# Kernel tuning notes

Hardware: AMD Instinct MI355X
Metric: run time of the kernel (lower is better)

The kernel has to match this reference:

```python
import jax, jax.numpy as jnp
import numpy as np

B, S, HID = 1, 2048, 2048
H, HD, DR = 16, 128, 64
CKV, CQ = 512, 1536
ROPE_BASE = 10000.0


def _rope_cos_sin(seq_len, dim, dtype):
    inv_freq = 1.0 / (ROPE_BASE ** (jnp.arange(0, dim, 2, dtype=jnp.float32) / dim))
    t = jnp.arange(seq_len, dtype=jnp.float32)
    freqs = jnp.outer(t, inv_freq)                      # [S, DR/2]
    emb = jnp.concatenate([freqs, freqs], axis=-1)      # [S, DR]
    return jnp.cos(emb).astype(dtype), jnp.sin(emb).astype(dtype)


def _rotate_half(x):
    x1, x2 = jnp.split(x, 2, axis=-1)
    return jnp.concatenate([-x2, x1], axis=-1)


def _xavier(key, fan_in, fan_out):
    lim = np.sqrt(6.0 / (fan_in + fan_out))
    return jax.random.uniform(key, (fan_in, fan_out), jnp.float32, -lim, lim)


def setup_inputs() -> dict:
    key = jax.random.key(0)
    ks = jax.random.split(key, 10)
    hidden_states = jax.random.normal(ks[0], (B, S, HID), jnp.float32)
    # causal mask: 1.0 where position is masked out (j > i)
    mask = jnp.triu(jnp.ones((S, S), jnp.float32), k=1)[None, None]  # [1,1,S,S]
    return {
        "hidden_states": hidden_states,
        "mask": mask,
        "W_DKV": _xavier(ks[1], HID, CKV),
        "W_UK": _xavier(ks[2], CKV, H * HD),
        "W_UV": _xavier(ks[3], CKV, H * HD),
        "W_DQ": _xavier(ks[4], HID, CQ),
        "W_UQ": _xavier(ks[5], CQ, H * HD),
        "W_QR": _xavier(ks[6], CQ, H * DR),
        "W_KR": _xavier(ks[7], HID, DR),
        "W_O": _xavier(ks[8], H * HD, HID),
    }


def reference(hidden_states, mask, W_DKV, W_UK, W_UV, W_DQ, W_UQ, W_QR, W_KR, W_O):
    b, s, _ = hidden_states.shape
    scale = 1.0 / np.sqrt(HD + DR)

    c_KV = hidden_states @ W_DKV                         # [B,S,CKV]
    k_C = (c_KV @ W_UK).reshape(b, s, H, HD)
    v = (c_KV @ W_UV).reshape(b, s, H, HD)
    c_Q = hidden_states @ W_DQ                           # [B,S,CQ]
    q_C = (c_Q @ W_UQ).reshape(b, s, H, HD)
    q_R = (c_Q @ W_QR).reshape(b, s, H, DR)
    k_R = (hidden_states @ W_KR).reshape(b, s, 1, DR)

    cos, sin = _rope_cos_sin(s, DR, hidden_states.dtype)
    cos = cos[None, :, None, :]                          # [1,S,1,DR]
    sin = sin[None, :, None, :]
    q_R = q_R * cos + _rotate_half(q_R) * sin
    k_R = k_R * cos + _rotate_half(k_R) * sin            # [B,S,1,DR], broadcast over heads

    q = jnp.concatenate([q_C, q_R], axis=-1)             # [B,S,H,HD+DR]
    k = jnp.concatenate([k_C, jnp.broadcast_to(k_R, (b, s, H, DR))], axis=-1)

    # [B,H,Sq,Sk]
    scores = jnp.einsum("bqhd,bkhd->bhqk", q, k) * scale
    if mask is not None:
        scores = scores + mask * -1e9                     # broadcast over heads
    probs = jax.nn.softmax(scores, axis=-1)
    out = jnp.einsum("bhqk,bkhd->bqhd", probs, v).reshape(b, s, H * HD)
    return out @ W_O
```

## Files before the change

### kernel.cpp

```cpp
#include <hip/hip_runtime.h>
#include <hip/hip_bf16.h>
#include <math.h>

typedef __hip_bfloat16 bf16;
typedef short s16x8 __attribute__((ext_vector_type(8)));
typedef unsigned short u16x8 __attribute__((ext_vector_type(8)));
typedef float f32x4 __attribute__((ext_vector_type(4)));

#define S_LEN 2048
#define NHEAD 16
#define HDIM  128
#define DROT  64

__device__ __forceinline__ float bf2f(unsigned short u) {
    union { unsigned int i; float f; } v;
    v.i = ((unsigned int)u) << 16;
    return v.f;
}
__device__ __forceinline__ unsigned short f2bf(float f) {
    union { float f; unsigned int i; } v;
    v.f = f;
    unsigned int r = (v.i + 0x7FFFu + ((v.i >> 16) & 1u)) >> 16;
    return (unsigned short)r;
}

__device__ __forceinline__ void load_lds16(const unsigned short* g, unsigned short* l) {
    __builtin_amdgcn_global_load_lds(
        (const __attribute__((address_space(1))) unsigned short*)g,
        (__attribute__((address_space(3))) unsigned short*)l, 16, 0, 0);
}

__device__ __forceinline__ bool is_bf16(const unsigned int* maskw) {
    return maskw[1] != 0x3F800000u;
}

struct PrepDesc {
    const void* in;
    unsigned short* out;
    int R, C, blk_start, nbx, kind;
};
struct PrepBatch { PrepDesc d[8]; };

__global__ __launch_bounds__(256)
void prep_kernel(PrepBatch b, const unsigned int* __restrict__ maskw) {
    const bool fb = is_bf16(maskw);
    __shared__ unsigned short t[64][80];
    PrepDesc dd = b.d[0];
    #pragma unroll
    for (int p = 1; p < 8; ++p)
        if ((int)blockIdx.x >= b.d[p].blk_start) dd = b.d[p];
    const int local = (int)blockIdx.x - dd.blk_start;
    const int tid = threadIdx.x;

    if (dd.kind == 1) {
        const size_t idx = ((size_t)local * 256 + tid) * 8;
        if (fb) {
            *(u16x8*)(dd.out + idx) = *(const u16x8*)((const unsigned short*)dd.in + idx);
        } else {
            const float* p = (const float*)dd.in + idx;
            float4 f0 = *(const float4*)p;
            float4 f1 = *(const float4*)(p + 4);
            u16x8 u;
            u[0] = f2bf(f0.x); u[1] = f2bf(f0.y); u[2] = f2bf(f0.z); u[3] = f2bf(f0.w);
            u[4] = f2bf(f1.x); u[5] = f2bf(f1.y); u[6] = f2bf(f1.z); u[7] = f2bf(f1.w);
            *(u16x8*)(dd.out + idx) = u;
        }
        return;
    }

    const int by = local / dd.nbx, bx = local - by * dd.nbx;
    const int r0 = by << 6, c0 = bx << 6;
    const int tr = tid >> 3;
    const int tc8 = (tid & 7) << 3;
    #pragma unroll
    for (int p = 0; p < 2; ++p) {
        const int r = tr + p * 32;
        const size_t off = (size_t)(r0 + r) * dd.C + c0 + tc8;
        unsigned short v[8];
        if (fb) {
            u16x8 u = *(const u16x8*)((const unsigned short*)dd.in + off);
            #pragma unroll
            for (int j = 0; j < 8; ++j) v[j] = u[j];
        } else {
            const float* p4 = (const float*)dd.in + off;
            float4 f0 = *(const float4*)p4;
            float4 f1 = *(const float4*)(p4 + 4);
            v[0] = f2bf(f0.x); v[1] = f2bf(f0.y); v[2] = f2bf(f0.z); v[3] = f2bf(f0.w);
            v[4] = f2bf(f1.x); v[5] = f2bf(f1.y); v[6] = f2bf(f1.z); v[7] = f2bf(f1.w);
        }
        #pragma unroll
        for (int j = 0; j < 8; ++j) t[tc8 + j][r] = v[j];
    }
    __syncthreads();
    #pragma unroll
    for (int p = 0; p < 2; ++p) {
        const int c = tr + p * 32;
        u16x8 u = *(const u16x8*)&t[c][tc8];
        *(u16x8*)(dd.out + (size_t)(c0 + c) * dd.R + r0 + tc8) = u;
    }
}

__global__ __launch_bounds__(256)
void transpose_conv(const void* __restrict__ in, unsigned short* __restrict__ out,
                    int R, int C, const unsigned int* __restrict__ maskw) {
    const bool fb = is_bf16(maskw);
    __shared__ unsigned short t[64][80];
    const int r0 = blockIdx.y << 6, c0 = blockIdx.x << 6;
    const int tid = threadIdx.x;
    const int tr = tid >> 3;
    const int tc8 = (tid & 7) << 3;
    #pragma unroll
    for (int p = 0; p < 2; ++p) {
        const int r = tr + p * 32;
        const size_t off = (size_t)(r0 + r) * C + c0 + tc8;
        unsigned short v[8];
        if (fb) {
            u16x8 u = *(const u16x8*)((const unsigned short*)in + off);
            #pragma unroll
            for (int j = 0; j < 8; ++j) v[j] = u[j];
        } else {
            const float* p4 = (const float*)in + off;
            float4 f0 = *(const float4*)p4;
            float4 f1 = *(const float4*)(p4 + 4);
            v[0] = f2bf(f0.x); v[1] = f2bf(f0.y); v[2] = f2bf(f0.z); v[3] = f2bf(f0.w);
            v[4] = f2bf(f1.x); v[5] = f2bf(f1.y); v[6] = f2bf(f1.z); v[7] = f2bf(f1.w);
        }
        #pragma unroll
        for (int j = 0; j < 8; ++j) t[tc8 + j][r] = v[j];
    }
    __syncthreads();
    #pragma unroll
    for (int p = 0; p < 2; ++p) {
        const int c = tr + p * 32;
        u16x8 u = *(const u16x8*)&t[c][tc8];
        *(u16x8*)(out + (size_t)(c0 + c) * R + r0 + tc8) = u;
    }
}

struct GemmDesc {
    const unsigned short* A;
    const unsigned short* Bt;
    void* C;
    int M, N, K;
    int nbx;
    int blk_start;
    int ct;
};
struct GemmBatch { GemmDesc d[4]; };

template <int NP, int CMODE>
__global__ __launch_bounds__(256)
void mfma_gemm2(GemmBatch batch, const unsigned int* __restrict__ maskw) {
    __shared__ __align__(16) unsigned short As[128 * 32];
    __shared__ __align__(16) unsigned short Bs[128 * 32];

    GemmDesc dd = batch.d[0];
    #pragma unroll
    for (int p = 1; p < NP; ++p)
        if ((int)blockIdx.x >= batch.d[p].blk_start) dd = batch.d[p];
    const int local = (int)blockIdx.x - dd.blk_start;
    const int by = local / dd.nbx;
    const int bx = local - by * dd.nbx;
    const int m0 = by << 7, n0 = bx << 7;
    const int K = dd.K;

    const int tid  = threadIdx.x;
    const int lane = tid & 63;
    const int w    = tid >> 6;
    const int wr = w >> 1, wc = w & 1;
    const int l15 = lane & 15, quad = lane >> 4, q8 = quad << 3;

    int srow[2], scol[2];
    #pragma unroll
    for (int i = 0; i < 2; ++i) {
        const int c = (2 * w + i) * 64 + lane;
        srow[i] = c >> 2;
        scol[i] = (c & 3) << 3;
    }

    f32x4 acc[4][4];
    #pragma unroll
    for (int i = 0; i < 4; ++i)
        #pragma unroll
        for (int j = 0; j < 4; ++j) {
            f32x4 z = {0.f, 0.f, 0.f, 0.f};
            acc[i][j] = z;
        }

    for (int k0 = 0; k0 < K; k0 += 32) {
        __syncthreads();
        #pragma unroll
        for (int i = 0; i < 2; ++i) {
            load_lds16(dd.A  + (size_t)(m0 + srow[i]) * K + k0 + scol[i],
                       As + (2 * w + i) * 512);
            load_lds16(dd.Bt + (size_t)(n0 + srow[i]) * K + k0 + scol[i],
                       Bs + (2 * w + i) * 512);
        }
        __syncthreads();
        s16x8 af[4], bf[4];
        #pragma unroll
        for (int mt = 0; mt < 4; ++mt)
            af[mt] = *(const s16x8*)&As[(wr * 64 + mt * 16 + l15) * 32 + q8];
        #pragma unroll
        for (int nt = 0; nt < 4; ++nt)
            bf[nt] = *(const s16x8*)&Bs[(wc * 64 + nt * 16 + l15) * 32 + q8];
        #pragma unroll
        for (int nt = 0; nt < 4; ++nt)
            #pragma unroll
            for (int mt = 0; mt < 4; ++mt)
                acc[mt][nt] = __builtin_amdgcn_mfma_f32_16x16x32_bf16(
                    af[mt], bf[nt], acc[mt][nt], 0, 0, 0);
    }

    bool cbf = true;
    if (CMODE == 2) cbf = is_bf16(maskw);
    const int M = dd.M, N = dd.N;
    #pragma unroll
    for (int mt = 0; mt < 4; ++mt)
        #pragma unroll
        for (int nt = 0; nt < 4; ++nt) {
            f32x4 d = acc[mt][nt];
            const int col  = n0 + wc * 64 + nt * 16 + l15;
            const int rowb = m0 + wr * 64 + mt * 16 + quad * 4;
            if (dd.ct) {
                ushort4 o;
                o.x = f2bf(d[0]); o.y = f2bf(d[1]); o.z = f2bf(d[2]); o.w = f2bf(d[3]);
                *(ushort4*)((unsigned short*)dd.C + (size_t)col * M + rowb) = o;
            } else if (cbf) {
                unsigned short* c = (unsigned short*)dd.C + (size_t)rowb * N + col;
                #pragma unroll
                for (int r = 0; r < 4; ++r) c[(size_t)r * N] = f2bf(d[r]);
            } else {
                float* c = (float*)dd.C + (size_t)rowb * N + col;
                #pragma unroll
                for (int r = 0; r < 4; ++r) c[(size_t)r * N] = d[r];
            }
        }
}

__global__ __launch_bounds__(256)
void rope_all(unsigned short* __restrict__ qR, unsigned short* __restrict__ kRb) {
    int bid = blockIdx.x;
    unsigned short* x;
    int nh, stride;
    if (bid < 4096) { x = qR; nh = 16; stride = 64; }
    else            { x = kRb; nh = 1; stride = 128; bid -= 4096; }
    const int idx = bid * 256 + threadIdx.x;
    const int d = idx & 31;
    const int rest = idx >> 5;
    const int h = rest % nh;
    const int s = rest / nh;
    if (s >= S_LEN) return;
    const float inv = powf(10000.0f, -(float)d * (1.0f / 32.0f));
    const float ang = (float)s * inv;
    float si, co;
    sincosf(ang, &si, &co);
    unsigned short* p = x + ((size_t)s * nh + h) * stride;
    const float x1 = bf2f(p[d]);
    const float x2 = bf2f(p[d + 32]);
    p[d]      = f2bf(x1 * co - x2 * si);
    p[d + 32] = f2bf(x2 * co + x1 * si);
}

__global__ __launch_bounds__(256)
void mfma_attn(const unsigned short* __restrict__ qC,
               const unsigned short* __restrict__ qR,
               const unsigned short* __restrict__ kC,
               const unsigned short* __restrict__ kRb,
               const unsigned short* __restrict__ vT,
               unsigned short* __restrict__ at) {
    __shared__ __align__(16) struct {
        unsigned short Ks[64][200];
        unsigned short Vs[128][72];
        unsigned short Ps[4][16][72];
    } sm;

    const int tid  = threadIdx.x;
    const int lane = tid & 63;
    const int w    = tid >> 6;
    const int l15 = lane & 15, quad = lane >> 4, q8 = quad << 3;

    const int bid  = (int)blockIdx.x;
    const int half = bid >> 8;
    const int idx  = bid & 255;
    const int h    = idx & 15;
    const int qh   = idx >> 4;
    const int qb   = half ? (31 - qh) : qh;
    const int q0 = qb << 6;
    const int qrow = q0 + w * 16 + l15;

    s16x8 qf[6];
    {
        const unsigned short* qCrow = qC + ((size_t)qrow * NHEAD + h) * HDIM;
        #pragma unroll
        for (int s = 0; s < 4; ++s)
            qf[s] = *(const s16x8*)(qCrow + s * 32 + q8);
        const unsigned short* qRrow = qR + ((size_t)qrow * NHEAD + h) * DROT;
        #pragma unroll
        for (int s = 0; s < 2; ++s)
            qf[4 + s] = *(const s16x8*)(qRrow + s * 32 + q8);
    }

    f32x4 accO[8];
    #pragma unroll
    for (int i = 0; i < 8; ++i) { f32x4 z = {0.f, 0.f, 0.f, 0.f}; accO[i] = z; }
    float slocal[4] = {0.f, 0.f, 0.f, 0.f};

    const float scale = 0.0721687836487032f;
    const int ntiles = (q0 >> 6) + 1;

    const int krow = tid >> 2, kcb = (tid & 3) * 48;
    const int vd = tid >> 1, vcb = (tid & 1) << 5;

    u16x8 kreg[6], vreg[4];
    {
        #pragma unroll
        for (int m = 0; m < 6; ++m) {
            const int c = kcb + m * 8;
            const unsigned short* src = (c < 128)
                ? kC + ((size_t)krow * NHEAD + h) * HDIM + c
                : kRb + (size_t)krow * 128 + (c - 128);
            kreg[m] = *(const u16x8*)src;
        }
        const unsigned short* vrow = vT + (size_t)(h * HDIM + vd) * S_LEN;
        #pragma unroll
        for (int m = 0; m < 4; ++m)
            vreg[m] = *(const u16x8*)(vrow + vcb + m * 8);
    }

    for (int t = 0; t < ntiles; ++t) {
        const int key0 = t << 6;
        __syncthreads();
        #pragma unroll
        for (int m = 0; m < 6; ++m)
            *(u16x8*)&sm.Ks[krow][kcb + m * 8] = kreg[m];
        #pragma unroll
        for (int m = 0; m < 4; ++m)
            *(u16x8*)&sm.Vs[vd][vcb + m * 8] = vreg[m];
        __syncthreads();

        if (t + 1 < ntiles) {
            const int kn = key0 + 64;
            #pragma unroll
            for (int m = 0; m < 6; ++m) {
                const int c = kcb + m * 8;
                const unsigned short* src = (c < 128)
                    ? kC + ((size_t)(kn + krow) * NHEAD + h) * HDIM + c
                    : kRb + (size_t)(kn + krow) * 128 + (c - 128);
                kreg[m] = *(const u16x8*)src;
            }
            const unsigned short* vrow = vT + (size_t)(h * HDIM + vd) * S_LEN + kn;
            #pragma unroll
            for (int m = 0; m < 4; ++m)
                vreg[m] = *(const u16x8*)(vrow + vcb + m * 8);
        }

        f32x4 sA[4];
        #pragma unroll
        for (int nt = 0; nt < 4; ++nt) { f32x4 z = {0.f, 0.f, 0.f, 0.f}; sA[nt] = z; }
        #pragma unroll
        for (int s = 0; s < 6; ++s)
            #pragma unroll
            for (int nt = 0; nt < 4; ++nt) {
                s16x8 kf = *(const s16x8*)&sm.Ks[nt * 16 + l15][s * 32 + q8];
                sA[nt] = __builtin_amdgcn_mfma_f32_16x16x32_bf16(qf[s], kf, sA[nt], 0, 0, 0);
            }

        const int rbase = q0 + w * 16 + quad * 4;
        const bool diag = (key0 + 63 > q0 + w * 16);
        float pv[4][4];
        #pragma unroll
        for (int nt = 0; nt < 4; ++nt) {
            const int col = key0 + nt * 16 + l15;
            #pragma unroll
            for (int r = 0; r < 4; ++r) {
                float s = sA[nt][r] * scale;
                if (diag && (col > rbase + r)) s = -1e30f;
                pv[nt][r] = __expf(s);
            }
        }
        #pragma unroll
        for (int r = 0; r < 4; ++r) {
            slocal[r] += (pv[0][r] + pv[1][r]) + (pv[2][r] + pv[3][r]);
            #pragma unroll
            for (int nt = 0; nt < 4; ++nt)
                sm.Ps[w][quad * 4 + r][nt * 16 + l15] = f2bf(pv[nt][r]);
        }

        s16x8 pf0 = *(const s16x8*)&sm.Ps[w][l15][q8];
        s16x8 pf1 = *(const s16x8*)&sm.Ps[w][l15][32 + q8];
        #pragma unroll
        for (int dt = 0; dt < 8; ++dt) {
            s16x8 vf0 = *(const s16x8*)&sm.Vs[dt * 16 + l15][q8];
            s16x8 vf1 = *(const s16x8*)&sm.Vs[dt * 16 + l15][32 + q8];
            accO[dt] = __builtin_amdgcn_mfma_f32_16x16x32_bf16(pf0, vf0, accO[dt], 0, 0, 0);
            accO[dt] = __builtin_amdgcn_mfma_f32_16x16x32_bf16(pf1, vf1, accO[dt], 0, 0, 0);
        }
    }

    float l_r[4];
    #pragma unroll
    for (int r = 0; r < 4; ++r) {
        float sum = slocal[r];
        #pragma unroll
        for (int off = 1; off < 16; off <<= 1)
            sum += __shfl_xor(sum, off, 64);
        l_r[r] = sum;
    }

    #pragma unroll
    for (int r = 0; r < 4; ++r) {
        const float linv = 1.f / l_r[r];
        const int row = q0 + w * 16 + quad * 4 + r;
        unsigned short* dst = at + (size_t)row * (NHEAD * HDIM) + h * HDIM + l15;
        #pragma unroll
        for (int dt = 0; dt < 8; ++dt)
            dst[dt * 16] = f2bf(accO[dt][r] * linv);
    }
}

extern "C" void kernel_launch(void* const* d_in, const int* in_sizes, int n_in,
                              void* d_out, int out_size, void* d_ws, size_t ws_size,
                              hipStream_t stream) {
    (void)in_sizes; (void)n_in; (void)out_size; (void)ws_size;

    const void* hs    = d_in[0];
    const unsigned int* maskw = (const unsigned int*)d_in[1];
    const void* W_DKV = d_in[2];
    const void* W_UK  = d_in[3];
    const void* W_UV  = d_in[4];
    const void* W_DQ  = d_in[5];
    const void* W_UQ  = d_in[6];
    const void* W_QR  = d_in[7];
    const void* W_KR  = d_in[8];
    const void* W_O   = d_in[9];

    const size_t M1 = 1048576;
    unsigned short* ws    = (unsigned short*)d_ws;
    unsigned short* cKV   = ws;
    unsigned short* cQ    = ws + 1 * M1;
    unsigned short* kC    = ws + 4 * M1;
    unsigned short* vT    = ws + 8 * M1;
    unsigned short* DKVt  = ws + 8 * M1;
    unsigned short* DQt   = ws + 9 * M1;
    unsigned short* qC    = ws + 12 * M1;
    unsigned short* hs_bf = ws + 12 * M1;
    unsigned short* qR    = ws + 16 * M1;
    unsigned short* kRb   = ws + 18 * M1;
    unsigned short* KRt   = ws + 18 * M1 + 262144;
    unsigned short* at    = ws + 18 * M1 + 524288;
    unsigned short* UKt   = at;
    unsigned short* UVt   = at + 1 * M1;
    unsigned short* QRt   = at + 2 * M1;
    unsigned short* UQt   = ws + 22 * M1 + 524288;
    unsigned short* WOt   = ws;

    const dim3 blk(256);

    {
        PrepBatch b{};
        b.d[0] = { hs,    hs_bf, 0, 0,           0,  0, 1 };
        b.d[1] = { W_DKV, DKVt,  2048,  512,  2048,  8, 0 };
        b.d[2] = { W_DQ,  DQt,   2048, 1536,  2304, 24, 0 };
        b.d[3] = { W_KR,  KRt,   2048,   64,  3072,  1, 0 };
        b.d[4] = { W_UK,  UKt,    512, 2048,  3104, 32, 0 };
        b.d[5] = { W_UV,  UVt,    512, 2048,  3360, 32, 0 };
        b.d[6] = { W_UQ,  UQt,   1536, 2048,  3616, 32, 0 };
        b.d[7] = { W_QR,  QRt,   1536, 1024,  4384, 16, 0 };
        prep_kernel<<<4768, blk, 0, stream>>>(b, maskw);
    }

    {
        GemmBatch b{};
        b.d[0] = { hs_bf, DQt,  (void*)cQ,  2048, 1536, 2048, 12,   0, 0 };
        b.d[1] = { hs_bf, DKVt, (void*)cKV, 2048,  512, 2048,  4, 192, 0 };
        b.d[2] = { hs_bf, KRt,  (void*)kRb, 2048,  128, 2048,  1, 256, 0 };
        b.d[3] = b.d[2];
        mfma_gemm2<3, 1><<<272, blk, 0, stream>>>(b, maskw);
    }

    {
        GemmBatch b{};
        b.d[0] = { cQ,  UQt, (void*)qC, 2048, 2048, 1536, 16,   0, 0 };
        b.d[1] = { cQ,  QRt, (void*)qR, 2048, 1024, 1536,  8, 256, 0 };
        b.d[2] = { cKV, UKt, (void*)kC, 2048, 2048,  512, 16, 384, 0 };
        b.d[3] = { cKV, UVt, (void*)vT, 2048, 2048,  512, 16, 640, 1 };
        mfma_gemm2<4, 1><<<896, blk, 0, stream>>>(b, maskw);
    }

    rope_all<<<4352, blk, 0, stream>>>(qR, kRb);

    transpose_conv<<<dim3(32, 32), blk, 0, stream>>>(W_O, WOt, 2048, 2048, maskw);

    mfma_attn<<<512, blk, 0, stream>>>(qC, qR, kC, kRb, vT, at);

    {
        GemmBatch b{};
        b.d[0] = { at, WOt, d_out, 2048, 2048, 2048, 16, 0, 0 };
        b.d[1] = b.d[0]; b.d[2] = b.d[0]; b.d[3] = b.d[0];
        mfma_gemm2<1, 2><<<256, blk, 0, stream>>>(b, maskw);
    }
}
```

Baseline: 356.4 us.

## Split attention waves 2x2 over query and key halves with LDS reduction

Reorganizes the attention block so each wave handles 32 query rows and 32 keys of every 64-key tile, instead of 16 rows against all 64 keys. Each K and V fragment read from LDS is now reused for two MFMAs, cutting LDS traffic per MFMA. Waves whose key half lies entirely above the causal diagonal skip that tile. The two key-half partial outputs and row sums are combined through a shared-memory union at the end, which adds an extra sync and a reduction pass and doubles the per-wave accumulator registers, possibly lowering occupancy.

Result: no change. 361.8 us (+1.5%).

```diff
diff --git a/kernel.cpp b/kernel.cpp
--- a/kernel.cpp
+++ b/kernel.cpp
@@ -269,42 +269,54 @@
                const unsigned short* __restrict__ kRb,
                const unsigned short* __restrict__ vT,
                unsigned short* __restrict__ at) {
-    __shared__ __align__(16) struct {
-        unsigned short Ks[64][200];
-        unsigned short Vs[128][72];
-        unsigned short Ps[4][16][72];
+    __shared__ __align__(16) union {
+        struct {
+            unsigned short Ks[64][200];
+            unsigned short Vs[128][72];
+            unsigned short Ps[4][32][40];
+        } s;
+        struct {
+            float O[2][32][132];
+            float L[2][32];
+        } m;
     } sm;
 
     const int tid  = threadIdx.x;
     const int lane = tid & 63;
     const int w    = tid >> 6;
+    const int qhw  = w & 1;
+    const int kh   = w >> 1;
     const int l15 = lane & 15, quad = lane >> 4, q8 = quad << 3;
 
     const int bid  = (int)blockIdx.x;
     const int half = bid >> 8;
     const int idx  = bid & 255;
     const int h    = idx & 15;
-    const int qh   = idx >> 4;
-    const int qb   = half ? (31 - qh) : qh;
-    const int q0 = qb << 6;
-    const int qrow = q0 + w * 16 + l15;
-
-    s16x8 qf[6];
-    {
+    const int qhh  = idx >> 4;
+    const int qb   = half ? (31 - qhh) : qhh;
+    const int q0   = qb << 6;
+    const int qrow0 = q0 + qhw * 32;
+
+    s16x8 qf[2][6];
+    #pragma unroll
+    for (int mt = 0; mt < 2; ++mt) {
+        const int qrow = qrow0 + mt * 16 + l15;
         const unsigned short* qCrow = qC + ((size_t)qrow * NHEAD + h) * HDIM;
         #pragma unroll
         for (int s = 0; s < 4; ++s)
-            qf[s] = *(const s16x8*)(qCrow + s * 32 + q8);
+            qf[mt][s] = *(const s16x8*)(qCrow + s * 32 + q8);
         const unsigned short* qRrow = qR + ((size_t)qrow * NHEAD + h) * DROT;
         #pragma unroll
         for (int s = 0; s < 2; ++s)
-            qf[4 + s] = *(const s16x8*)(qRrow + s * 32 + q8);
-    }
-
-    f32x4 accO[8];
-    #pragma unroll
-    for (int i = 0; i < 8; ++i) { f32x4 z = {0.f, 0.f, 0.f, 0.f}; accO[i] = z; }
-    float slocal[4] = {0.f, 0.f, 0.f, 0.f};
+            qf[mt][4 + s] = *(const s16x8*)(qRrow + s * 32 + q8);
+    }
+
+    f32x4 accO[2][8];
+    #pragma unroll
+    for (int mt = 0; mt < 2; ++mt)
+        #pragma unroll
+        for (int i = 0; i < 8; ++i) { f32x4 z = {0.f, 0.f, 0.f, 0.f}; accO[mt][i] = z; }
+    float slocal[2][4] = {{0.f, 0.f, 0.f, 0.f}, {0.f, 0.f, 0.f, 0.f}};
 
     const float scale = 0.0721687836487032f;
     const int ntiles = (q0 >> 6) + 1;
@@ -333,10 +345,10 @@
         __syncthreads();
         #pragma unroll
         for (int m = 0; m < 6; ++m)
-            *(u16x8*)&sm.Ks[krow][kcb + m * 8] = kreg[m];
+            *(u16x8*)&sm.s.Ks[krow][kcb + m * 8] = kreg[m];
         #pragma unroll
         for (int m = 0; m < 4; ++m)
-            *(u16x8*)&sm.Vs[vd][vcb + m * 8] = vreg[m];
+            *(u16x8*)&sm.s.Vs[vd][vcb + m * 8] = vreg[m];
         __syncthreads();
 
         if (t + 1 < ntiles) {
@@ -355,67 +367,106 @@
                 vreg[m] = *(const u16x8*)(vrow + vcb + m * 8);
         }
 
-        f32x4 sA[4];
-        #pragma unroll
-        for (int nt = 0; nt < 4; ++nt) { f32x4 z = {0.f, 0.f, 0.f, 0.f}; sA[nt] = z; }
-        #pragma unroll
-        for (int s = 0; s < 6; ++s)
-            #pragma unroll
-            for (int nt = 0; nt < 4; ++nt) {
-                s16x8 kf = *(const s16x8*)&sm.Ks[nt * 16 + l15][s * 32 + q8];
-                sA[nt] = __builtin_amdgcn_mfma_f32_16x16x32_bf16(qf[s], kf, sA[nt], 0, 0, 0);
+        const int wk0 = key0 + kh * 32;
+        const bool active = wk0 <= qrow0 + 31;
+        if (active) {
+            f32x4 sA[2][2];
+            #pragma unroll
+            for (int mt = 0; mt < 2; ++mt)
+                #pragma unroll
+                for (int nt = 0; nt < 2; ++nt) { f32x4 z = {0.f, 0.f, 0.f, 0.f}; sA[mt][nt] = z; }
+            #pragma unroll
+            for (int s = 0; s < 6; ++s)
+                #pragma unroll
+                for (int nt = 0; nt < 2; ++nt) {
+                    s16x8 kf = *(const s16x8*)&sm.s.Ks[kh * 32 + nt * 16 + l15][s * 32 + q8];
+                    #pragma unroll
+                    for (int mt = 0; mt < 2; ++mt)
+                        sA[mt][nt] = __builtin_amdgcn_mfma_f32_16x16x32_bf16(
+                            qf[mt][s], kf, sA[mt][nt], 0, 0, 0);
+                }
+
+            #pragma unroll
+            for (int mt = 0; mt < 2; ++mt) {
+                const int rbase = qrow0 + mt * 16 + quad * 4;
+                const bool diag = (wk0 + 31 > qrow0 + mt * 16);
+                #pragma unroll
+                for (int nt = 0; nt < 2; ++nt) {
+                    const int col = wk0 + nt * 16 + l15;
+                    #pragma unroll
+                    for (int r = 0; r < 4; ++r) {
+                        float s = sA[mt][nt][r] * scale;
+                        if (diag && (col > rbase + r)) s = -1e30f;
+                        const float p = __expf(s);
+                        slocal[mt][r] += p;
+                        sm.s.Ps[w][mt * 16 + quad * 4 + r][nt * 16 + l15] = f2bf(p);
+                    }
+                }
             }
 
-        const int rbase = q0 + w * 16 + quad * 4;
-        const bool diag = (key0 + 63 > q0 + w * 16);
-        float pv[4][4];
-        #pragma unroll
-        for (int nt = 0; nt < 4; ++nt) {
-            const int col = key0 + nt * 16 + l15;
+            s16x8 pf[2];
+            #pragma unroll
+            for (int mt = 0; mt < 2; ++mt)
+                pf[mt] = *(const s16x8*)&sm.s.Ps[w][mt * 16 + l15][q8];
+            #pragma unroll
+            for (int dt = 0; dt < 8; ++dt) {
+                s16x8 vf = *(const s16x8*)&sm.s.Vs[dt * 16 + l15][kh * 32 + q8];
+                #pragma unroll
+                for (int mt = 0; mt < 2; ++mt)
+                    accO[mt][dt] = __builtin_amdgcn_mfma_f32_16x16x32_bf16(
+                        pf[mt], vf, accO[mt][dt], 0, 0, 0);
+            }
+        }
+    }
+
+    float l_r[2][4];
+    #pragma unroll
+    for (int mt = 0; mt < 2; ++mt)
+        #pragma unroll
+        for (int r = 0; r < 4; ++r) {
+            float sum = slocal[mt][r];
+            #pragma unroll
+            for (int off = 1; off < 16; off <<= 1)
+                sum += __shfl_xor(sum, off, 64);
+            l_r[mt][r] = sum;
+        }
+
+    __syncthreads();
+    if (kh == 1) {
+        #pragma unroll
+        for (int mt = 0; mt < 2; ++mt) {
+            #pragma unroll
+            for (int dt = 0; dt < 8; ++dt)
+                #pragma unroll
+                for (int r = 0; r < 4; ++r)
+                    sm.m.O[qhw][mt * 16 + quad * 4 + r][dt * 16 + l15] = accO[mt][dt][r];
+            if (l15 == 0)
+                #pragma unroll
+                for (int r = 0; r < 4; ++r)
+                    sm.m.L[qhw][mt * 16 + quad * 4 + r] = l_r[mt][r];
+        }
+    }
+    __syncthreads();
+    if (kh == 0) {
+        #pragma unroll
+        for (int mt = 0; mt < 2; ++mt) {
+            const float lsum0 = l_r[mt][0] + sm.m.L[qhw][mt * 16 + quad * 4 + 0];
+            const float lsum1 = l_r[mt][1] + sm.m.L[qhw][mt * 16 + quad * 4 + 1];
+            const float lsum2 = l_r[mt][2] + sm.m.L[qhw][mt * 16 + quad * 4 + 2];
+            const float lsum3 = l_r[mt][3] + sm.m.L[qhw][mt * 16 + quad * 4 + 3];
+            const float linv[4] = { 1.f / lsum0, 1.f / lsum1, 1.f / lsum2, 1.f / lsum3 };
             #pragma unroll
             for (int r = 0; r < 4; ++r) {
-                float s = sA[nt][r] * scale;
-                if (diag && (col > rbase + r)) s = -1e30f;
-                pv[nt][r] = __expf(s);
+                const int row = qrow0 + mt * 16 + quad * 4 + r;
+                unsigned short* dst = at + (size_t)row * (NHEAD * HDIM) + h * HDIM + l15;
+                #pragma unroll
+                for (int dt = 0; dt < 8; ++dt) {
+                    const float o = accO[mt][dt][r]
+                                  + sm.m.O[qhw][mt * 16 + quad * 4 + r][dt * 16 + l15];
+                    dst[dt * 16] = f2bf(o * linv[r]);
+                }
             }
         }
-        #pragma unroll
-        for (int r = 0; r < 4; ++r) {
-            slocal[r] += (pv[0][r] + pv[1][r]) + (pv[2][r] + pv[3][r]);
-            #pragma unroll
-            for (int nt = 0; nt < 4; ++nt)
-                sm.Ps[w][quad * 4 + r][nt * 16 + l15] = f2bf(pv[nt][r]);
-        }
-
-        s16x8 pf0 = *(const s16x8*)&sm.Ps[w][l15][q8];
-        s16x8 pf1 = *(const s16x8*)&sm.Ps[w][l15][32 + q8];
-        #pragma unroll
-        for (int dt = 0; dt < 8; ++dt) {
-            s16x8 vf0 = *(const s16x8*)&sm.Vs[dt * 16 + l15][q8];
-            s16x8 vf1 = *(const s16x8*)&sm.Vs[dt * 16 + l15][32 + q8];
-            accO[dt] = __builtin_amdgcn_mfma_f32_16x16x32_bf16(pf0, vf0, accO[dt], 0, 0, 0);
-            accO[dt] = __builtin_amdgcn_mfma_f32_16x16x32_bf16(pf1, vf1, accO[dt], 0, 0, 0);
-        }
-    }
-
-    float l_r[4];
-    #pragma unroll
-    for (int r = 0; r < 4; ++r) {
-        float sum = slocal[r];
-        #pragma unroll
-        for (int off = 1; off < 16; off <<= 1)
-            sum += __shfl_xor(sum, off, 64);
-        l_r[r] = sum;
-    }
-
-    #pragma unroll
-    for (int r = 0; r < 4; ++r) {
-        const float linv = 1.f / l_r[r];
-        const int row = q0 + w * 16 + quad * 4 + r;
-        unsigned short* dst = at + (size_t)row * (NHEAD * HDIM) + h * HDIM + l15;
-        #pragma unroll
-        for (int dt = 0; dt < 8; ++dt)
-            dst[dt * 16] = f2bf(accO[dt][r] * linv);
     }
 }
 
```

## Split attention key tile across two wave groups with shared-memory merge

Applied to the files above, without the earlier changes.

The attention block grows from 4 to 8 waves. Each query stripe is now handled by two waves, each taking one 32-key half of the 64-key tile. Waves whose key half lies entirely above the causal diagonal skip their MMA and exp work. At the end, the partial output accumulators and row sums from the second wave group are written to a union'd shared-memory buffer and added into the first group's results before normalization. This doubles the waves available to hide latency and reduces per-thread load and register work, at the cost of an extra reduction pass through LDS and more threads contending for the same barriers.

Result: faster. 343.6 us (-3.6%).

```diff
diff --git a/kernel.cpp b/kernel.cpp
--- a/kernel.cpp
+++ b/kernel.cpp
@@ -262,35 +262,44 @@
     p[d + 32] = f2bf(x2 * co + x1 * si);
 }
 
-__global__ __launch_bounds__(256)
+__global__ __launch_bounds__(512)
 void mfma_attn(const unsigned short* __restrict__ qC,
                const unsigned short* __restrict__ qR,
                const unsigned short* __restrict__ kC,
                const unsigned short* __restrict__ kRb,
                const unsigned short* __restrict__ vT,
                unsigned short* __restrict__ at) {
-    __shared__ __align__(16) struct {
-        unsigned short Ks[64][200];
-        unsigned short Vs[128][72];
-        unsigned short Ps[4][16][72];
+    __shared__ __align__(16) union {
+        struct {
+            unsigned short Ks[64][200];
+            unsigned short Vs[128][72];
+            unsigned short Ps[8][16][40];
+        } s;
+        struct {
+            float O[4][16][132];
+            float L[4][16];
+        } m;
     } sm;
 
     const int tid  = threadIdx.x;
     const int lane = tid & 63;
     const int w    = tid >> 6;
+    const int qs   = w & 3;
+    const int kh   = w >> 2;
     const int l15 = lane & 15, quad = lane >> 4, q8 = quad << 3;
 
     const int bid  = (int)blockIdx.x;
     const int half = bid >> 8;
     const int idx  = bid & 255;
     const int h    = idx & 15;
-    const int qh   = idx >> 4;
-    const int qb   = half ? (31 - qh) : qh;
-    const int q0 = qb << 6;
-    const int qrow = q0 + w * 16 + l15;
+    const int qhh  = idx >> 4;
+    const int qb   = half ? (31 - qhh) : qhh;
+    const int q0   = qb << 6;
+    const int qrow0 = q0 + qs * 16;
 
     s16x8 qf[6];
     {
+        const int qrow = qrow0 + l15;
         const unsigned short* qCrow = qC + ((size_t)qrow * NHEAD + h) * HDIM;
         #pragma unroll
         for (int s = 0; s < 4; ++s)
@@ -309,13 +318,15 @@
     const float scale = 0.0721687836487032f;
     const int ntiles = (q0 >> 6) + 1;
 
-    const int krow = tid >> 2, kcb = (tid & 3) * 48;
-    const int vd = tid >> 1, vcb = (tid & 1) << 5;
-
-    u16x8 kreg[6], vreg[4];
+    const int krow = tid >> 3;
+    const int kcb  = (tid & 7) * 24;
+    const int vd   = tid >> 2;
+    const int vcb  = (tid & 3) << 4;
+
+    u16x8 kreg[3], vreg[2];
     {
         #pragma unroll
-        for (int m = 0; m < 6; ++m) {
+        for (int m = 0; m < 3; ++m) {
             const int c = kcb + m * 8;
             const unsigned short* src = (c < 128)
                 ? kC + ((size_t)krow * NHEAD + h) * HDIM + c
@@ -324,7 +335,7 @@
         }
         const unsigned short* vrow = vT + (size_t)(h * HDIM + vd) * S_LEN;
         #pragma unroll
-        for (int m = 0; m < 4; ++m)
+        for (int m = 0; m < 2; ++m)
             vreg[m] = *(const u16x8*)(vrow + vcb + m * 8);
     }
 
@@ -332,17 +343,17 @@
         const int key0 = t << 6;
         __syncthreads();
         #pragma unroll
-        for (int m = 0; m < 6; ++m)
-            *(u16x8*)&sm.Ks[krow][kcb + m * 8] = kreg[m];
-        #pragma unroll
-        for (int m = 0; m < 4; ++m)
-            *(u16x8*)&sm.Vs[vd][vcb + m * 8] = vreg[m];
+        for (int m = 0; m < 3; ++m)
+            *(u16x8*)&sm.s.Ks[krow][kcb + m * 8] = kreg[m];
+        #pragma unroll
+        for (int m = 0; m < 2; ++m)
+            *(u16x8*)&sm.s.Vs[vd][vcb + m * 8] = vreg[m];
         __syncthreads();
 
         if (t + 1 < ntiles) {
             const int kn = key0 + 64;
             #pragma unroll
-            for (int m = 0; m < 6; ++m) {
+            for (int m = 0; m < 3; ++m) {
                 const int c = kcb + m * 8;
                 const unsigned short* src = (c < 128)
                     ? kC + ((size_t)(kn + krow) * NHEAD + h) * HDIM + c
@@ -351,50 +362,45 @@
             }
             const unsigned short* vrow = vT + (size_t)(h * HDIM + vd) * S_LEN + kn;
             #pragma unroll
-            for (int m = 0; m < 4; ++m)
+            for (int m = 0; m < 2; ++m)
                 vreg[m] = *(const u16x8*)(vrow + vcb + m * 8);
         }
 
-        f32x4 sA[4];
-        #pragma unroll
-        for (int nt = 0; nt < 4; ++nt) { f32x4 z = {0.f, 0.f, 0.f, 0.f}; sA[nt] = z; }
-        #pragma unroll
-        for (int s = 0; s < 6; ++s)
-            #pragma unroll
-            for (int nt = 0; nt < 4; ++nt) {
-                s16x8 kf = *(const s16x8*)&sm.Ks[nt * 16 + l15][s * 32 + q8];
-                sA[nt] = __builtin_amdgcn_mfma_f32_16x16x32_bf16(qf[s], kf, sA[nt], 0, 0, 0);
+        const int wk0 = key0 + kh * 32;
+        const bool active = wk0 <= qrow0 + 15;
+        if (active) {
+            f32x4 sA[2];
+            #pragma unroll
+            for (int nt = 0; nt < 2; ++nt) { f32x4 z = {0.f, 0.f, 0.f, 0.f}; sA[nt] = z; }
+            #pragma unroll
+            for (int s = 0; s < 6; ++s)
+                #pragma unroll
+                for (int nt = 0; nt < 2; ++nt) {
+                    s16x8 kf = *(const s16x8*)&sm.s.Ks[kh * 32 + nt * 16 + l15][s * 32 + q8];
+                    sA[nt] = __builtin_amdgcn_mfma_f32_16x16x32_bf16(qf[s], kf, sA[nt], 0, 0, 0);
+                }
+
+            const int rbase = qrow0 + quad * 4;
+            const bool diag = (wk0 + 31 > qrow0);
+            #pragma unroll
+            for (int nt = 0; nt < 2; ++nt) {
+                const int col = wk0 + nt * 16 + l15;
+                #pragma unroll
+                for (int r = 0; r < 4; ++r) {
+                    float s = sA[nt][r] * scale;
+                    if (diag && (col > rbase + r)) s = -1e30f;
+                    const float p = __expf(s);
+                    slocal[r] += p;
+                    sm.s.Ps[w][quad * 4 + r][nt * 16 + l15] = f2bf(p);
+                }
             }
 
-        const int rbase = q0 + w * 16 + quad * 4;
-        const bool diag = (key0 + 63 > q0 + w * 16);
-        float pv[4][4];
-        #pragma unroll
-        for (int nt = 0; nt < 4; ++nt) {
-            const int col = key0 + nt * 16 + l15;
-            #pragma unroll
-            for (int r = 0; r < 4; ++r) {
-                float s = sA[nt][r] * scale;
-                if (diag && (col > rbase + r)) s = -1e30f;
-                pv[nt][r] = __expf(s);
+            s16x8 pf = *(const s16x8*)&sm.s.Ps[w][l15][q8];
+            #pragma unroll
+            for (int dt = 0; dt < 8; ++dt) {
+                s16x8 vf = *(const s16x8*)&sm.s.Vs[dt * 16 + l15][kh * 32 + q8];
+                accO[dt] = __builtin_amdgcn_mfma_f32_16x16x32_bf16(pf, vf, accO[dt], 0, 0, 0);
             }
-        }
-        #pragma unroll
-        for (int r = 0; r < 4; ++r) {
-            slocal[r] += (pv[0][r] + pv[1][r]) + (pv[2][r] + pv[3][r]);
-            #pragma unroll
-            for (int nt = 0; nt < 4; ++nt)
-                sm.Ps[w][quad * 4 + r][nt * 16 + l15] = f2bf(pv[nt][r]);
-        }
-
-        s16x8 pf0 = *(const s16x8*)&sm.Ps[w][l15][q8];
-        s16x8 pf1 = *(const s16x8*)&sm.Ps[w][l15][32 + q8];
-        #pragma unroll
-        for (int dt = 0; dt < 8; ++dt) {
-            s16x8 vf0 = *(const s16x8*)&sm.Vs[dt * 16 + l15][q8];
-            s16x8 vf1 = *(const s16x8*)&sm.Vs[dt * 16 + l15][32 + q8];
-            accO[dt] = __builtin_amdgcn_mfma_f32_16x16x32_bf16(pf0, vf0, accO[dt], 0, 0, 0);
-            accO[dt] = __builtin_amdgcn_mfma_f32_16x16x32_bf16(pf1, vf1, accO[dt], 0, 0, 0);
         }
     }
 
@@ -408,14 +414,35 @@
         l_r[r] = sum;
     }
 
-    #pragma unroll
-    for (int r = 0; r < 4; ++r) {
-        const float linv = 1.f / l_r[r];
-        const int row = q0 + w * 16 + quad * 4 + r;
-        unsigned short* dst = at + (size_t)row * (NHEAD * HDIM) + h * HDIM + l15;
+    __syncthreads();
+    if (kh == 1) {
         #pragma unroll
         for (int dt = 0; dt < 8; ++dt)
-            dst[dt * 16] = f2bf(accO[dt][r] * linv);
+            #pragma unroll
+            for (int r = 0; r < 4; ++r)
+                sm.m.O[qs][quad * 4 + r][dt * 16 + l15] = accO[dt][r];
+        if (l15 == 0)
+            #pragma unroll
+            for (int r = 0; r < 4; ++r)
+                sm.m.L[qs][quad * 4 + r] = l_r[r];
+    }
+    __syncthreads();
+    if (kh == 0) {
+        float linv[4];
+        #pragma unroll
+        for (int r = 0; r < 4; ++r)
+            linv[r] = 1.f / (l_r[r] + sm.m.L[qs][quad * 4 + r]);
+        #pragma unroll
+        for (int r = 0; r < 4; ++r) {
+            const int row = qrow0 + quad * 4 + r;
+            unsigned short* dst = at + (size_t)row * (NHEAD * HDIM) + h * HDIM + l15;
+            #pragma unroll
+            for (int dt = 0; dt < 8; ++dt) {
+                const float o = accO[dt][r]
+                              + sm.m.O[qs][quad * 4 + r][dt * 16 + l15];
+                dst[dt * 16] = f2bf(o * linv[r]);
+            }
+        }
     }
 }
 
@@ -492,7 +519,7 @@
 
     transpose_conv<<<dim3(32, 32), blk, 0, stream>>>(W_O, WOt, 2048, 2048, maskw);
 
-    mfma_attn<<<512, blk, 0, stream>>>(qC, qR, kC, kRb, vT, at);
+    mfma_attn<<<512, dim3(512), 0, stream>>>(qC, qR, kC, kRb, vT, at);
 
     {
         GemmBatch b{};
```
